# Kernel optimization log

Hardware: AMD Instinct MI355X
Metric: run time of the kernel (lower is better)

## Reference

```python
import jax, jax.numpy as jnp
import numpy as np

N = 10000   # num nodes
E = 640000  # num edges
D_IN, D_HID, D_OUT = 128, 256, 128


def _cheb_layer(x, src, dst, dis, W0, W1, b):
    """PyG ChebConv with K=2, sym norm, lambda_max=2.0 (no edge weights):
    out = x @ W0 + (L_hat x) @ W1 + b, with L_hat = -D^{-1/2} A D^{-1/2}."""
    norm = -(dis[src] * dis[dst])                       # [E]
    msg = norm[:, None] * x[src]                        # [E, d]
    tx1 = jax.ops.segment_sum(msg, dst, num_segments=N)  # [N, d]
    return x @ W0 + tx1 @ W1 + b


def setup_inputs() -> dict:
    key = jax.random.key(0)
    ks = jax.random.split(key, 10)

    def glorot(k, fan_in, fan_out):
        s = jnp.sqrt(6.0 / (fan_in + fan_out))
        return jax.random.uniform(k, (fan_in, fan_out), jnp.float32, -s, s)

    x = jax.random.normal(ks[0], (N, D_IN), jnp.float32)
    edge_index = jax.random.randint(ks[1], (2, E), 0, N, jnp.int64)
    edge_type = jax.random.randint(ks[2], (E,), 0, 5, jnp.int64)
    return {
        "x": x,
        "edge_index": edge_index,
        "edge_type": edge_type,
        "W01": glorot(ks[3], D_IN, D_HID),
        "W11": glorot(ks[4], D_IN, D_HID),
        "b1": jnp.zeros((D_HID,), jnp.float32),
        "W02": glorot(ks[5], D_HID, D_HID),
        "W12": glorot(ks[6], D_HID, D_HID),
        "b2": jnp.zeros((D_HID,), jnp.float32),
        "W03": glorot(ks[7], D_HID, D_OUT),
        "W13": glorot(ks[8], D_HID, D_OUT),
        "b3": jnp.zeros((D_OUT,), jnp.float32),
    }


def reference(x, edge_index, edge_type, W01, W11, b1, W02, W12, b2, W03, W13, b3):
    # edge_type is unused by ChebConv (matches the original forward signature).
    src, dst = edge_index[0], edge_index[1]
    deg = jax.ops.segment_sum(jnp.ones((E,), x.dtype), src, num_segments=N)
    dis = jnp.where(deg > 0, jax.lax.rsqrt(jnp.maximum(deg, 1.0)), 0.0)
    # eval mode: dropout(p=0.4) is identity
    h = jax.nn.relu(_cheb_layer(x, src, dst, dis, W01, W11, b1))
    h = jax.nn.relu(_cheb_layer(h, src, dst, dis, W02, W12, b2))
    return _cheb_layer(h, src, dst, dis, W03, W13, b3)
```

## Files before the change

### kernel.cpp

```cpp
#include <hip/hip_runtime.h>

#define D_IN 128
#define D_HID 256
#define D_OUT 128
#define NBIN 10240
#define HB 256

typedef __attribute__((ext_vector_type(8))) unsigned short ushort8v;
typedef __attribute__((ext_vector_type(4))) unsigned short ushort4v;
typedef __attribute__((ext_vector_type(8))) short short8v;
typedef __attribute__((ext_vector_type(4))) float f32x4;

__device__ __forceinline__ unsigned short f2bf(float f) {
    unsigned u = __float_as_uint(f);
    unsigned r = (u + 0x7fffu + ((u >> 16) & 1u)) >> 16;
    return (unsigned short)r;
}
__device__ __forceinline__ float bf2f(unsigned short b) {
    return __uint_as_float((unsigned)b << 16);
}


__global__ __launch_bounds__(256) void k_hist(const int* __restrict__ src, const int* __restrict__ dst,
                                              unsigned short* __restrict__ psrc,
                                              unsigned short* __restrict__ pdst,
                                              int E, int EPB) {
    __shared__ int h[NBIN];
    int b = blockIdx.x, t = threadIdx.x;
    const int* arr = blockIdx.y ? dst : src;
    unsigned short* outp = blockIdx.y ? pdst : psrc;
    for (int i = t; i < NBIN; i += 256) h[i] = 0;
    __syncthreads();
    int beg = b * EPB, end = beg + EPB; if (end > E) end = E;
    for (int e = beg + t; e < end; e += 256)
        atomicAdd(&h[arr[e]], 1);
    __syncthreads();
    for (int i = t; i < NBIN; i += 256)
        outp[(size_t)b * NBIN + i] = (unsigned short)h[i];
}


__global__ __launch_bounds__(256) void k_colsum(const unsigned short* __restrict__ psrc,
                                                unsigned short* __restrict__ pdst,
                                                float* __restrict__ dis, int* __restrict__ cnt) {
    int bin = blockIdx.x * 256 + threadIdx.x;
    if (bin >= NBIN) return;
    int degs = 0;
    for (int b = 0; b < HB; ++b) degs += psrc[(size_t)b * NBIN + bin];
    int c = 0;
    for (int b = 0; b < HB; ++b) {
        int v = pdst[(size_t)b * NBIN + bin];
        pdst[(size_t)b * NBIN + bin] = (unsigned short)c;
        c += v;
    }
    dis[bin] = degs > 0 ? rsqrtf((float)degs) : 0.f;
    cnt[bin] = c;
}


__global__ void k_scan(const int* __restrict__ cnt, int* __restrict__ off, int n, int E) {
    __shared__ int sums[256];
    int t = threadIdx.x;
    int chunk = (n + 255) / 256;
    int beg = t * chunk;
    int end = beg + chunk; if (end > n) end = n;
    int s = 0;
    for (int i = beg; i < end; ++i) s += cnt[i];
    sums[t] = s;
    __syncthreads();
    if (t == 0) {
        int running = 0;
        for (int i = 0; i < 256; ++i) { int tmp = sums[i]; sums[i] = running; running += tmp; }
        off[n] = E;
    }
    __syncthreads();
    int pre = sums[t];
    for (int i = beg; i < end; ++i) { off[i] = pre; pre += cnt[i]; }
}


__global__ __launch_bounds__(256) void k_scatter2(const int* __restrict__ src, const int* __restrict__ dst,
                                                  const float* __restrict__ dis, const int* __restrict__ off,
                                                  const unsigned short* __restrict__ pfx,
                                                  unsigned* __restrict__ edges, int E, int EPB) {
    __shared__ int lcnt[NBIN];
    int b = blockIdx.x, t = threadIdx.x;
    for (int i = t; i < NBIN; i += 256) lcnt[i] = 0;
    __syncthreads();
    int beg = b * EPB, end = beg + EPB; if (end > E) end = E;
    const unsigned short* pf = pfx + (size_t)b * NBIN;
    for (int e = beg + t; e < end; e += 256) {
        int s = src[e], d = dst[e];
        int r = atomicAdd(&lcnt[d], 1);
        int pos = off[d] + (int)pf[d] + r;
        float nv = -(dis[s] * dis[d]);
        edges[pos] = ((unsigned)s << 16) | (unsigned)f2bf(nv);
    }
}


struct WtrArgs {
    const float* W[6];
    unsigned short* T[6];
    int K[6];
    int N[6];
    const float* xin;
    unsigned short* xout;
    int nElem;
};

__global__ __launch_bounds__(256) void k_wtr7(WtrArgs args) {
    __shared__ float tile[32][33];
    int z = blockIdx.z;
    if (z == 6) {
        int bid = blockIdx.y * 8 + blockIdx.x;
        int stride = 64 * 256 * 4;
        for (int i = (bid * 256 + threadIdx.x) * 4; i < args.nElem; i += stride) {
            float4 v = *reinterpret_cast<const float4*>(&args.xin[i]);
            ushort4v o;
            o[0] = f2bf(v.x); o[1] = f2bf(v.y); o[2] = f2bf(v.z); o[3] = f2bf(v.w);
            *reinterpret_cast<ushort4v*>(&args.xout[i]) = o;
        }
        return;
    }
    const float* W = args.W[z];
    unsigned short* Wt = args.T[z];
    int K = args.K[z], N = args.N[z];
    int k0 = blockIdx.x * 32, n0 = blockIdx.y * 32;
    if (k0 >= K || n0 >= N) return;
    int tx = threadIdx.x & 31, ty = threadIdx.x >> 5;
    for (int i = ty; i < 32; i += 8) tile[i][tx] = W[(size_t)(k0 + i) * N + n0 + tx];
    __syncthreads();
    for (int i = ty; i < 32; i += 8) Wt[(size_t)(n0 + i) * K + k0 + tx] = f2bf(tile[tx][i]);
}


#define AGG_GATHER(eSet, vSet)                                                        \
    _Pragma("unroll")                                                                 \
    for (int u = 0; u < 8; ++u)                                                       \
        vSet[u] = *reinterpret_cast<const ushort8v*>(&xb[(size_t)(eSet[u] >> 16) * D + cbase]);

#define AGG_ACCUM(eSet, vSet)                                                         \
    _Pragma("unroll")                                                                 \
    for (int u = 0; u < 8; ++u) {                                                     \
        float nv = __uint_as_float(eSet[u] << 16);                                    \
        _Pragma("unroll")                                                             \
        for (int j = 0; j < 8; ++j)                                                   \
            acc[j] += nv * bf2f(vSet[u][j]);                                          \
    }

template<int D, bool STBF, bool STF32, bool ADDB>
__global__ __launch_bounds__(256) void k_agg_bf(const int* __restrict__ off,
                                                const unsigned* __restrict__ edges,
                                                const unsigned short* __restrict__ xb,
                                                unsigned short* __restrict__ outb,
                                                float* __restrict__ outf,
                                                const float* __restrict__ base, int n) {
    const int CHUNK = 128;
    const int TPN = CHUNK / 8;
    const int NPB = 256 / TPN;
    int tid = threadIdx.x;
    int node = blockIdx.x * NPB + tid / TPN;
    if (node >= n) return;
    int cbase = blockIdx.y * CHUNK + (tid % TPN) * 8;
    int i = off[node], end = off[node + 1];
    float acc[8] = {};
    int nb = (end - i) >> 3;

    if (nb > 0) {
        unsigned e0[8], e1[8];
        ushort8v v0[8], v1[8];
        #pragma unroll
        for (int u = 0; u < 8; ++u) e0[u] = edges[i + u];
        AGG_GATHER(e0, v0)
        int b = 1;
        for (; b + 1 < nb; b += 2) {
            int base1 = i + b * 8;
            #pragma unroll
            for (int u = 0; u < 8; ++u) e1[u] = edges[base1 + u];
            AGG_GATHER(e1, v1)
            AGG_ACCUM(e0, v0)
            int base0 = i + (b + 1) * 8;
            #pragma unroll
            for (int u = 0; u < 8; ++u) e0[u] = edges[base0 + u];
            AGG_GATHER(e0, v0)
            AGG_ACCUM(e1, v1)
        }
        if (b < nb) {
            int base1 = i + b * 8;
            #pragma unroll
            for (int u = 0; u < 8; ++u) e1[u] = edges[base1 + u];
            AGG_GATHER(e1, v1)
            AGG_ACCUM(e0, v0)
            AGG_ACCUM(e1, v1)
        } else {
            AGG_ACCUM(e0, v0)
        }
    }
    for (int t = i + nb * 8; t < end; ++t) {
        unsigned e = edges[t];
        float nv = __uint_as_float(e << 16);
        ushort8v v = *reinterpret_cast<const ushort8v*>(&xb[(size_t)(e >> 16) * D + cbase]);
        #pragma unroll
        for (int j = 0; j < 8; ++j)
            acc[j] += nv * bf2f(v[j]);
    }

    if (ADDB) {
        float4 b0 = *reinterpret_cast<const float4*>(&base[(size_t)node * D + cbase]);
        float4 b1 = *reinterpret_cast<const float4*>(&base[(size_t)node * D + cbase + 4]);
        acc[0] += b0.x; acc[1] += b0.y; acc[2] += b0.z; acc[3] += b0.w;
        acc[4] += b1.x; acc[5] += b1.y; acc[6] += b1.z; acc[7] += b1.w;
    }
    if (STBF) {
        ushort8v ob;
        #pragma unroll
        for (int j = 0; j < 8; ++j) ob[j] = f2bf(acc[j]);
        *reinterpret_cast<ushort8v*>(&outb[(size_t)node * D + cbase]) = ob;
    }
    if (STF32) {
        float4 o0, o1;
        o0.x = acc[0]; o0.y = acc[1]; o0.z = acc[2]; o0.w = acc[3];
        o1.x = acc[4]; o1.y = acc[5]; o1.z = acc[6]; o1.w = acc[7];
        *reinterpret_cast<float4*>(&outf[(size_t)node * D + cbase]) = o0;
        *reinterpret_cast<float4*>(&outf[(size_t)node * D + cbase + 4]) = o1;
    }
}


#define LDT 72

template<int K, bool RELU, bool HAS_B2, bool HAS_BIAS, bool ST_BF, bool ST_F32>
__global__ __launch_bounds__(256) void k_gemm_mfma(
        const unsigned short* __restrict__ A1, const unsigned short* __restrict__ W0t,
        const unsigned short* __restrict__ A2, const unsigned short* __restrict__ W1t,
        const float* __restrict__ bias,
        float* __restrict__ C, unsigned short* __restrict__ Cb, int M, int N) {
    __shared__ unsigned short As[64 * LDT];
    __shared__ unsigned short Bs[128 * LDT];
    int tid = threadIdx.x, lane = tid & 63, wave = tid >> 6;
    int wm = wave >> 1, wn = wave & 1;
    int row0 = blockIdx.x * 64, col0 = blockIdx.y * 128;
    f32x4 acc[2][4];
    #pragma unroll
    for (int i = 0; i < 2; ++i)
        #pragma unroll
        for (int j = 0; j < 4; ++j)
            acc[i][j] = (f32x4){0.f, 0.f, 0.f, 0.f};

    int aRow = wm * 32 + (lane & 15);
    int bRow = wn * 64 + (lane & 15);
    int kOff = (lane >> 4) * 8;
    int sr = tid >> 2, sc = (tid & 3) * 8;
    int gra = row0 + sr; if (gra >= M) gra = M - 1;

    const int npass = HAS_B2 ? 2 : 1;
    for (int pass = 0; pass < npass; ++pass) {
        const unsigned short* A = pass ? A2 : A1;
        const unsigned short* W = pass ? W1t : W0t;
        for (int k0 = 0; k0 < K; k0 += 64) {
            #pragma unroll
            for (int h = 0; h < 2; ++h) {
                ushort8v va = *reinterpret_cast<const ushort8v*>(&A[(size_t)gra * K + k0 + sc + h * 32]);
                *reinterpret_cast<ushort8v*>(&As[sr * LDT + sc + h * 32]) = va;
            }
            #pragma unroll
            for (int g = 0; g < 2; ++g)
                #pragma unroll
                for (int h = 0; h < 2; ++h) {
                    int r = sr + g * 64;
                    ushort8v vb = *reinterpret_cast<const ushort8v*>(&W[(size_t)(col0 + r) * K + k0 + sc + h * 32]);
                    *reinterpret_cast<ushort8v*>(&Bs[r * LDT + sc + h * 32]) = vb;
                }
            __syncthreads();
            #pragma unroll
            for (int kk = 0; kk < 2; ++kk) {
                int ko = kOff + kk * 32;
                short8v a[2], bb[4];
                #pragma unroll
                for (int i = 0; i < 2; ++i)
                    a[i] = *reinterpret_cast<const short8v*>(&As[(aRow + i * 16) * LDT + ko]);
                #pragma unroll
                for (int i = 0; i < 4; ++i)
                    bb[i] = *reinterpret_cast<const short8v*>(&Bs[(bRow + i * 16) * LDT + ko]);
                #pragma unroll
                for (int mi = 0; mi < 2; ++mi)
                    #pragma unroll
                    for (int ni = 0; ni < 4; ++ni)
                        acc[mi][ni] = __builtin_amdgcn_mfma_f32_16x16x32_bf16(a[mi], bb[ni], acc[mi][ni], 0, 0, 0);
            }
            __syncthreads();
        }
    }

    int colBase = col0 + wn * 64 + (lane & 15);
    int rowSub = (lane >> 4) * 4;
    #pragma unroll
    for (int mi = 0; mi < 2; ++mi) {
        int rowF = row0 + wm * 32 + mi * 16 + rowSub;
        #pragma unroll
        for (int r = 0; r < 4; ++r) {
            int gr = rowF + r;
            if (gr < M) {
                #pragma unroll
                for (int ni = 0; ni < 4; ++ni) {
                    int gc = colBase + ni * 16;
                    float v = acc[mi][ni][r];
                    if (HAS_BIAS) v += bias[gc];
                    if (RELU)     v = fmaxf(v, 0.f);
                    if (ST_F32)   C[(size_t)gr * N + gc] = v;
                    if (ST_BF)    Cb[(size_t)gr * N + gc] = f2bf(v);
                }
            }
        }
    }
}


template<int K>
__global__ __launch_bounds__(256) void k_gemm_dual(
        const unsigned short* __restrict__ A1, const unsigned short* __restrict__ W03t,
        const unsigned short* __restrict__ W13t, const float* __restrict__ bias,
        float* __restrict__ part, unsigned short* __restrict__ y3b, int M) {
    const int N = 128;
    __shared__ unsigned short As[64 * LDT];
    __shared__ unsigned short Bs[128 * LDT];
    int tid = threadIdx.x, lane = tid & 63, wave = tid >> 6;
    int wm = wave >> 1, wn = wave & 1;
    int row0 = blockIdx.x * 64;
    const unsigned short* W = blockIdx.y ? W13t : W03t;
    f32x4 acc[2][4];
    #pragma unroll
    for (int i = 0; i < 2; ++i)
        #pragma unroll
        for (int j = 0; j < 4; ++j)
            acc[i][j] = (f32x4){0.f, 0.f, 0.f, 0.f};

    int aRow = wm * 32 + (lane & 15);
    int bRow = wn * 64 + (lane & 15);
    int kOff = (lane >> 4) * 8;
    int sr = tid >> 2, sc = (tid & 3) * 8;
    int gra = row0 + sr; if (gra >= M) gra = M - 1;

    for (int k0 = 0; k0 < K; k0 += 64) {
        #pragma unroll
        for (int h = 0; h < 2; ++h) {
            ushort8v va = *reinterpret_cast<const ushort8v*>(&A1[(size_t)gra * K + k0 + sc + h * 32]);
            *reinterpret_cast<ushort8v*>(&As[sr * LDT + sc + h * 32]) = va;
        }
        #pragma unroll
        for (int g = 0; g < 2; ++g)
            #pragma unroll
            for (int h = 0; h < 2; ++h) {
                int r = sr + g * 64;
                ushort8v vb = *reinterpret_cast<const ushort8v*>(&W[(size_t)r * K + k0 + sc + h * 32]);
                *reinterpret_cast<ushort8v*>(&Bs[r * LDT + sc + h * 32]) = vb;
            }
        __syncthreads();
        #pragma unroll
        for (int kk = 0; kk < 2; ++kk) {
            int ko = kOff + kk * 32;
            short8v a[2], bb[4];
            #pragma unroll
            for (int i = 0; i < 2; ++i)
                a[i] = *reinterpret_cast<const short8v*>(&As[(aRow + i * 16) * LDT + ko]);
            #pragma unroll
            for (int i = 0; i < 4; ++i)
                bb[i] = *reinterpret_cast<const short8v*>(&Bs[(bRow + i * 16) * LDT + ko]);
            #pragma unroll
            for (int mi = 0; mi < 2; ++mi)
                #pragma unroll
                for (int ni = 0; ni < 4; ++ni)
                    acc[mi][ni] = __builtin_amdgcn_mfma_f32_16x16x32_bf16(a[mi], bb[ni], acc[mi][ni], 0, 0, 0);
        }
        __syncthreads();
    }

    int colBase = wn * 64 + (lane & 15);
    int rowSub = (lane >> 4) * 4;
    bool isPart = (blockIdx.y == 0);
    #pragma unroll
    for (int mi = 0; mi < 2; ++mi) {
        int rowF = row0 + wm * 32 + mi * 16 + rowSub;
        #pragma unroll
        for (int r = 0; r < 4; ++r) {
            int gr = rowF + r;
            if (gr < M) {
                #pragma unroll
                for (int ni = 0; ni < 4; ++ni) {
                    int gc = colBase + ni * 16;
                    float v = acc[mi][ni][r];
                    if (isPart) part[(size_t)gr * N + gc] = v + bias[gc];
                    else        y3b[(size_t)gr * N + gc] = f2bf(v);
                }
            }
        }
    }
}


extern "C" void kernel_launch(void* const* d_in, const int* in_sizes, int n_in,
                              void* d_out, int out_size, void* d_ws, size_t ws_size,
                              hipStream_t stream) {
    const float* x   = (const float*)d_in[0];
    const int*   ei  = (const int*)d_in[1];
    const float* W01 = (const float*)d_in[3];
    const float* W11 = (const float*)d_in[4];
    const float* b1  = (const float*)d_in[5];
    const float* W02 = (const float*)d_in[6];
    const float* W12 = (const float*)d_in[7];
    const float* b2  = (const float*)d_in[8];
    const float* W03 = (const float*)d_in[9];
    const float* W13 = (const float*)d_in[10];
    const float* b3  = (const float*)d_in[11];
    float* out = (float*)d_out;

    const int n = in_sizes[0] / D_IN;
    const int E = in_sizes[1] / 2;
    const int* src = ei;
    const int* dst = ei + E;
    const int EPB = (E + HB - 1) / HB;

    char* wsb = (char*)d_ws;
    float* dis   = (float*)wsb;                   wsb += NBIN * 4;
    int*   cnt   = (int*)wsb;                     wsb += NBIN * 4;
    int*   off   = (int*)wsb;                     wsb += (NBIN + 16) * 4;
    unsigned short* psrc = (unsigned short*)wsb;  wsb += (size_t)HB * NBIN * 2;
    unsigned short* pdst = (unsigned short*)wsb;  wsb += (size_t)HB * NBIN * 2;
    unsigned* edges = (unsigned*)wsb;             wsb += (size_t)E * 4;
    unsigned short* txb  = (unsigned short*)wsb;  wsb += (size_t)n * D_HID * 2;
    float*          part = (float*)wsb;           wsb += (size_t)n * D_OUT * 4;
    unsigned short* x_bf = (unsigned short*)wsb;  wsb += (size_t)n * D_IN * 2;
    unsigned short* h1_bf = (unsigned short*)wsb; wsb += (size_t)n * D_HID * 2;
    unsigned short* h2_bf = (unsigned short*)wsb; wsb += (size_t)n * D_HID * 2;
    unsigned short* y3_bf = (unsigned short*)wsb; wsb += (size_t)n * D_OUT * 2;
    unsigned short* W01t = (unsigned short*)wsb;  wsb += (size_t)D_IN  * D_HID * 2;
    unsigned short* W11t = (unsigned short*)wsb;  wsb += (size_t)D_IN  * D_HID * 2;
    unsigned short* W02t = (unsigned short*)wsb;  wsb += (size_t)D_HID * D_HID * 2;
    unsigned short* W12t = (unsigned short*)wsb;  wsb += (size_t)D_HID * D_HID * 2;
    unsigned short* W03t = (unsigned short*)wsb;  wsb += (size_t)D_HID * D_OUT * 2;
    unsigned short* W13t = (unsigned short*)wsb;  wsb += (size_t)D_HID * D_OUT * 2;

    const int gmx = (n + 63) / 64;
    const int gax = (n + 15) / 16;

    k_hist<<<dim3(HB, 2), 256, 0, stream>>>(src, dst, psrc, pdst, E, EPB);
    k_colsum<<<NBIN / 256, 256, 0, stream>>>(psrc, pdst, dis, cnt);
    k_scan<<<1, 256, 0, stream>>>(cnt, off, n, E);
    k_scatter2<<<HB, 256, 0, stream>>>(src, dst, dis, off, pdst, edges, E, EPB);

    {
        WtrArgs wa;
        wa.W[0] = W01; wa.T[0] = W01t; wa.K[0] = D_IN;  wa.N[0] = D_HID;
        wa.W[1] = W11; wa.T[1] = W11t; wa.K[1] = D_IN;  wa.N[1] = D_HID;
        wa.W[2] = W02; wa.T[2] = W02t; wa.K[2] = D_HID; wa.N[2] = D_HID;
        wa.W[3] = W12; wa.T[3] = W12t; wa.K[3] = D_HID; wa.N[3] = D_HID;
        wa.W[4] = W03; wa.T[4] = W03t; wa.K[4] = D_HID; wa.N[4] = D_OUT;
        wa.W[5] = W13; wa.T[5] = W13t; wa.K[5] = D_HID; wa.N[5] = D_OUT;
        wa.xin = x; wa.xout = x_bf; wa.nElem = n * D_IN;
        k_wtr7<<<dim3(8, 8, 7), 256, 0, stream>>>(wa);
    }

    k_agg_bf<D_IN, true, false, false><<<dim3(gax, 1), 256, 0, stream>>>(
        off, edges, x_bf, txb, nullptr, nullptr, n);
    k_gemm_mfma<D_IN, true, true, true, true, false><<<dim3(gmx, D_HID / 128), 256, 0, stream>>>(
        x_bf, W01t, txb, W11t, b1, nullptr, h1_bf, n, D_HID);

    k_agg_bf<D_HID, true, false, false><<<dim3(gax, 2), 256, 0, stream>>>(
        off, edges, h1_bf, txb, nullptr, nullptr, n);
    k_gemm_mfma<D_HID, true, true, true, true, false><<<dim3(gmx, D_HID / 128), 256, 0, stream>>>(
        h1_bf, W02t, txb, W12t, b2, nullptr, h2_bf, n, D_HID);

    k_gemm_dual<D_HID><<<dim3(gmx, 2), 256, 0, stream>>>(
        h2_bf, W03t, W13t, b3, part, y3_bf, n);
    k_agg_bf<D_OUT, false, true, true><<<dim3(gax, 1), 256, 0, stream>>>(
        off, edges, y3_bf, nullptr, out, part, n);
}
```

Baseline: 169.9 us.

## Sort aggregation nodes by in-degree and fold weight transpose into hist kernel

```diff
diff --git a/kernel.cpp b/kernel.cpp
--- a/kernel.cpp
+++ b/kernel.cpp
@@ -21,12 +21,47 @@
 }
 
 
+struct WtrArgs {
+    const float* W[6];
+    unsigned short* T[6];
+    int K[6];
+    int N[6];
+    const float* xin;
+    unsigned short* xout;
+    int nElem;
+};
+
+
 __global__ __launch_bounds__(256) void k_hist(const int* __restrict__ src, const int* __restrict__ dst,
                                               unsigned short* __restrict__ psrc,
                                               unsigned short* __restrict__ pdst,
-                                              int E, int EPB) {
+                                              int E, int EPB, WtrArgs wa) {
     __shared__ int h[NBIN];
     int b = blockIdx.x, t = threadIdx.x;
+    if (blockIdx.y == 2) {
+        const int starts[7] = {0, 32, 64, 128, 192, 224, 256};
+        int m = 0;
+        while (b >= starts[m + 1]) ++m;
+        int local = b - starts[m];
+        int K = wa.K[m], N = wa.N[m];
+        int kt = K / 32;
+        int k0 = (local % kt) * 32, n0 = (local / kt) * 32;
+        float (*tile)[33] = (float(*)[33])h;
+        int tx = t & 31, ty = t >> 5;
+        const float* W = wa.W[m];
+        unsigned short* Wt = wa.T[m];
+        for (int i = ty; i < 32; i += 8) tile[i][tx] = W[(size_t)(k0 + i) * N + n0 + tx];
+        __syncthreads();
+        for (int i = ty; i < 32; i += 8) Wt[(size_t)(n0 + i) * K + k0 + tx] = f2bf(tile[tx][i]);
+        int stride = HB * 256 * 4;
+        for (int i = (b * 256 + t) * 4; i < wa.nElem; i += stride) {
+            float4 v = *reinterpret_cast<const float4*>(&wa.xin[i]);
+            ushort4v o;
+            o[0] = f2bf(v.x); o[1] = f2bf(v.y); o[2] = f2bf(v.z); o[3] = f2bf(v.w);
+            *reinterpret_cast<ushort4v*>(&wa.xout[i]) = o;
+        }
+        return;
+    }
     const int* arr = blockIdx.y ? dst : src;
     unsigned short* outp = blockIdx.y ? pdst : psrc;
     for (int i = t; i < NBIN; i += 256) h[i] = 0;
@@ -58,8 +93,10 @@
 }
 
 
-__global__ void k_scan(const int* __restrict__ cnt, int* __restrict__ off, int n, int E) {
+__global__ void k_scan(const int* __restrict__ cnt, int* __restrict__ off,
+                       int* __restrict__ perm, int n, int E) {
     __shared__ int sums[256];
+    __shared__ int dh[1024];
     int t = threadIdx.x;
     int chunk = (n + 255) / 256;
     int beg = t * chunk;
@@ -67,6 +104,7 @@
     int s = 0;
     for (int i = beg; i < end; ++i) s += cnt[i];
     sums[t] = s;
+    for (int i = t; i < 1024; i += 256) dh[i] = 0;
     __syncthreads();
     if (t == 0) {
         int running = 0;
@@ -75,7 +113,22 @@
     }
     __syncthreads();
     int pre = sums[t];
-    for (int i = beg; i < end; ++i) { off[i] = pre; pre += cnt[i]; }
+    for (int i = beg; i < end; ++i) {
+        off[i] = pre; pre += cnt[i];
+        int d = cnt[i]; if (d > 1023) d = 1023;
+        atomicAdd(&dh[d], 1);
+    }
+    __syncthreads();
+    if (t == 0) {
+        int r = 0;
+        for (int i = 0; i < 1024; ++i) { int v = dh[i]; dh[i] = r; r += v; }
+    }
+    __syncthreads();
+    for (int i = beg; i < end; ++i) {
+        int d = cnt[i]; if (d > 1023) d = 1023;
+        int rank = atomicAdd(&dh[d], 1);
+        perm[n - 1 - rank] = i;
+    }
 }
 
 
@@ -99,42 +152,6 @@
 }
 
 
-struct WtrArgs {
-    const float* W[6];
-    unsigned short* T[6];
-    int K[6];
-    int N[6];
-    const float* xin;
-    unsigned short* xout;
-    int nElem;
-};
-
-__global__ __launch_bounds__(256) void k_wtr7(WtrArgs args) {
-    __shared__ float tile[32][33];
-    int z = blockIdx.z;
-    if (z == 6) {
-        int bid = blockIdx.y * 8 + blockIdx.x;
-        int stride = 64 * 256 * 4;
-        for (int i = (bid * 256 + threadIdx.x) * 4; i < args.nElem; i += stride) {
-            float4 v = *reinterpret_cast<const float4*>(&args.xin[i]);
-            ushort4v o;
-            o[0] = f2bf(v.x); o[1] = f2bf(v.y); o[2] = f2bf(v.z); o[3] = f2bf(v.w);
-            *reinterpret_cast<ushort4v*>(&args.xout[i]) = o;
-        }
-        return;
-    }
-    const float* W = args.W[z];
-    unsigned short* Wt = args.T[z];
-    int K = args.K[z], N = args.N[z];
-    int k0 = blockIdx.x * 32, n0 = blockIdx.y * 32;
-    if (k0 >= K || n0 >= N) return;
-    int tx = threadIdx.x & 31, ty = threadIdx.x >> 5;
-    for (int i = ty; i < 32; i += 8) tile[i][tx] = W[(size_t)(k0 + i) * N + n0 + tx];
-    __syncthreads();
-    for (int i = ty; i < 32; i += 8) Wt[(size_t)(n0 + i) * K + k0 + tx] = f2bf(tile[tx][i]);
-}
-
-
 #define AGG_GATHER(eSet, vSet)                                                        \
     _Pragma("unroll")                                                                 \
     for (int u = 0; u < 8; ++u)                                                       \
@@ -151,6 +168,7 @@
 
 template<int D, bool STBF, bool STF32, bool ADDB>
 __global__ __launch_bounds__(256) void k_agg_bf(const int* __restrict__ off,
+                                                const int* __restrict__ perm,
                                                 const unsigned* __restrict__ edges,
                                                 const unsigned short* __restrict__ xb,
                                                 unsigned short* __restrict__ outb,
@@ -160,8 +178,9 @@
     const int TPN = CHUNK / 8;
     const int NPB = 256 / TPN;
     int tid = threadIdx.x;
-    int node = blockIdx.x * NPB + tid / TPN;
-    if (node >= n) return;
+    int g = blockIdx.x * NPB + tid / TPN;
+    if (g >= n) return;
+    int node = perm[g];
     int cbase = blockIdx.y * CHUNK + (tid % TPN) * 8;
     int i = off[node], end = off[node + 1];
     float acc[8] = {};
@@ -425,6 +444,7 @@
     float* dis   = (float*)wsb;                   wsb += NBIN * 4;
     int*   cnt   = (int*)wsb;                     wsb += NBIN * 4;
     int*   off   = (int*)wsb;                     wsb += (NBIN + 16) * 4;
+    int*   perm  = (int*)wsb;                     wsb += NBIN * 4;
     unsigned short* psrc = (unsigned short*)wsb;  wsb += (size_t)HB * NBIN * 2;
     unsigned short* pdst = (unsigned short*)wsb;  wsb += (size_t)HB * NBIN * 2;
     unsigned* edges = (unsigned*)wsb;             wsb += (size_t)E * 4;
@@ -444,35 +464,32 @@
     const int gmx = (n + 63) / 64;
     const int gax = (n + 15) / 16;
 
-    k_hist<<<dim3(HB, 2), 256, 0, stream>>>(src, dst, psrc, pdst, E, EPB);
+    WtrArgs wa;
+    wa.W[0] = W01; wa.T[0] = W01t; wa.K[0] = D_IN;  wa.N[0] = D_HID;
+    wa.W[1] = W11; wa.T[1] = W11t; wa.K[1] = D_IN;  wa.N[1] = D_HID;
+    wa.W[2] = W02; wa.T[2] = W02t; wa.K[2] = D_HID; wa.N[2] = D_HID;
+    wa.W[3] = W12; wa.T[3] = W12t; wa.K[3] = D_HID; wa.N[3] = D_HID;
+    wa.W[4] = W03; wa.T[4] = W03t; wa.K[4] = D_HID; wa.N[4] = D_OUT;
+    wa.W[5] = W13; wa.T[5] = W13t; wa.K[5] = D_HID; wa.N[5] = D_OUT;
+    wa.xin = x; wa.xout = x_bf; wa.nElem = n * D_IN;
+
+    k_hist<<<dim3(HB, 3), 256, 0, stream>>>(src, dst, psrc, pdst, E, EPB, wa);
     k_colsum<<<NBIN / 256, 256, 0, stream>>>(psrc, pdst, dis, cnt);
-    k_scan<<<1, 256, 0, stream>>>(cnt, off, n, E);
+    k_scan<<<1, 256, 0, stream>>>(cnt, off, perm, n, E);
     k_scatter2<<<HB, 256, 0, stream>>>(src, dst, dis, off, pdst, edges, E, EPB);
 
-    {
-        WtrArgs wa;
-        wa.W[0] = W01; wa.T[0] = W01t; wa.K[0] = D_IN;  wa.N[0] = D_HID;
-        wa.W[1] = W11; wa.T[1] = W11t; wa.K[1] = D_IN;  wa.N[1] = D_HID;
-        wa.W[2] = W02; wa.T[2] = W02t; wa.K[2] = D_HID; wa.N[2] = D_HID;
-        wa.W[3] = W12; wa.T[3] = W12t; wa.K[3] = D_HID; wa.N[3] = D_HID;
-        wa.W[4] = W03; wa.T[4] = W03t; wa.K[4] = D_HID; wa.N[4] = D_OUT;
-        wa.W[5] = W13; wa.T[5] = W13t; wa.K[5] = D_HID; wa.N[5] = D_OUT;
-        wa.xin = x; wa.xout = x_bf; wa.nElem = n * D_IN;
-        k_wtr7<<<dim3(8, 8, 7), 256, 0, stream>>>(wa);
-    }
-
     k_agg_bf<D_IN, true, false, false><<<dim3(gax, 1), 256, 0, stream>>>(
-        off, edges, x_bf, txb, nullptr, nullptr, n);
+        off, perm, edges, x_bf, txb, nullptr, nullptr, n);
     k_gemm_mfma<D_IN, true, true, true, true, false><<<dim3(gmx, D_HID / 128), 256, 0, stream>>>(
         x_bf, W01t, txb, W11t, b1, nullptr, h1_bf, n, D_HID);
 
     k_agg_bf<D_HID, true, false, false><<<dim3(gax, 2), 256, 0, stream>>>(
-        off, edges, h1_bf, txb, nullptr, nullptr, n);
+        off, perm, edges, h1_bf, txb, nullptr, nullptr, n);
     k_gemm_mfma<D_HID, true, true, true, true, false><<<dim3(gmx, D_HID / 128), 256, 0, stream>>>(
         h1_bf, W02t, txb, W12t, b2, nullptr, h2_bf, n, D_HID);
 
     k_gemm_dual<D_HID><<<dim3(gmx, 2), 256, 0, stream>>>(
         h2_bf, W03t, W13t, b3, part, y3_bf, n);
     k_agg_bf<D_OUT, false, true, true><<<dim3(gax, 1), 256, 0, stream>>>(
-        off, edges, y3_bf, nullptr, out, part, n);
-}
+        off, perm, edges, y3_bf, nullptr, out, part, n);
+}
```

Result: slower. 177.0 us (+4.2%).
